# Performance work log

Measured on AMD Instinct MI355X. Metric: run time of the kernel, lower is better.

Reference implementation:

```python
import jax, jax.numpy as jnp
import numpy as np

B, N, IN, E, OUT = 4, 128, 256, 128, 128
EPS = 1e-5
NEG = -1.0e9


def _ln(x, s, o):
    m = x.mean(-1, keepdims=True)
    v = ((x - m) ** 2).mean(-1, keepdims=True)
    return s * jax.lax.rsqrt(v + EPS) * (x - m) + o


def setup_inputs() -> dict:
    key = jax.random.key(0)
    ks = jax.random.split(key, 30)

    def w(k, i, o):
        return (jax.random.normal(k, (i, o), jnp.float32) / np.sqrt(i)).astype(jnp.float32)

    z_dense = jax.random.normal(ks[0], (B, N, IN), jnp.float32)
    e_dense = jax.random.normal(ks[1], (B, N, N, E), jnp.float32)
    graph_fts = jax.random.normal(ks[2], (B, IN // 2), jnp.float32)
    lengths = jax.random.randint(ks[3], (B,), N // 2, N + 1)
    mask = jnp.arange(N)[None, :] < lengths[:, None]  # (B,N) bool
    adj = jax.random.uniform(ks[4], (B, N, N)) < 0.3
    adj = (adj | jnp.eye(N, dtype=bool)[None]) & mask[:, :, None] & mask[:, None, :]
    return dict(
        z_dense=z_dense, e_dense=e_dense, graph_fts=graph_fts, mask=mask, adj_mat=adj,
        Wt1=w(ks[5], IN, 8), Wt2=w(ks[6], IN, 8), Wt3=w(ks[7], IN, 8),
        We1=w(ks[8], E, 8), We2=w(ks[9], E, 8), We3=w(ks[10], E, 8),
        Wg=w(ks[11], IN // 2, 8),
        Wm1=w(ks[12], IN, OUT), Wm2=w(ks[13], IN, OUT), Wme=w(ks[14], E, OUT), Wmg=w(ks[15], E, OUT),
        ln1_s=jnp.ones((OUT,), jnp.float32), ln1_o=jnp.zeros((OUT,), jnp.float32),
        Wmlp1=w(ks[16], OUT, OUT),
        ln2_s=jnp.ones((OUT,), jnp.float32), ln2_o=jnp.zeros((OUT,), jnp.float32),
        Wmlp2=w(ks[17], OUT, OUT),
        WU1=w(ks[18], IN, OUT), WU2=w(ks[19], OUT, OUT), WU3=w(ks[20], 8, OUT),
        lnf_s=jnp.ones((OUT,), jnp.float32), lnf_o=jnp.zeros((OUT,), jnp.float32),
    )


def reference(z_dense, e_dense, graph_fts, mask, adj_mat,
              Wt1, Wt2, Wt3, We1, We2, We3, Wg,
              Wm1, Wm2, Wme, Wmg,
              ln1_s, ln1_o, Wmlp1, ln2_s, ln2_o, Wmlp2,
              WU1, WU2, WU3, lnf_s, lnf_o):
    mN = mask[..., None]  # (B,N,1)
    # --- triplet messages ---
    tri_1 = jnp.where(mN, z_dense @ Wt1, 0.0)  # (B,N,8)
    tri_2 = jnp.where(mN, z_dense @ Wt2, 0.0)
    tri_3 = jnp.where(mN, z_dense @ Wt3, 0.0)
    tri_e1 = e_dense @ We1  # (B,N,N,8)
    tri_e2 = e_dense @ We2
    tri_e3 = e_dense @ We3
    tri_g = graph_fts @ Wg  # (B,8)
    # (B,N,N,N,8) 7-way broadcast sum (axes: b, i, j, k)
    tri = (tri_1[:, :, None, None, :] + tri_2[:, None, :, None, :] + tri_3[:, None, None, :, :]
           + tri_e1[:, :, :, None, :] + tri_e2[:, :, None, :, :] + tri_e3[:, None, :, :, :]
           + tri_g[:, None, None, None, :])
    msk_tri = mask[:, None, None, :] | mask[:, None, :, None] | mask[:, :, None, None]
    tri = jnp.where(msk_tri[..., None], tri, NEG)
    tri_pooled = tri.max(axis=1)  # (B,N,N,8) -- max over first node axis
    tri_msgs = jax.nn.relu(tri_pooled @ WU3)  # (B,N,N,OUT)

    # --- pairwise messages ---
    msg_1 = jnp.where(mN, z_dense @ Wm1, 0.0)  # (B,N,OUT)
    msg_2 = jnp.where(mN, z_dense @ Wm2, 0.0)
    msg_e = jnp.where(adj_mat[..., None], e_dense @ Wme, 0.0)  # (B,N,N,OUT)
    msg_g = graph_fts @ Wmg  # (B,OUT)
    msgs = msg_1[:, None, :, :] + msg_2[:, :, None, :] + msg_e + msg_g[:, None, None, :]
    # M[-1]: [LN, ReLU, Linear] x2
    x = jax.nn.relu(_ln(msgs, ln1_s, ln1_o)) @ Wmlp1
    x = jax.nn.relu(_ln(x, ln2_s, ln2_o)) @ Wmlp2
    msgs = jnp.where(adj_mat[..., None], x, NEG).max(axis=1)  # (B,N,OUT)

    ret = _ln(z_dense @ WU1 + msgs @ WU2, lnf_s, lnf_o)  # (B,N,OUT)
    return ret, msgs, tri_msgs
```

## Files before the change

### kernel.cpp

```cpp
#include <hip/hip_runtime.h>

#define BN   4
#define NN   128
#define INF  256
#define EF   128
#define OUTF 128
#define EPSF 1e-5f
#define NEGF -998244352.0f

typedef __attribute__((ext_vector_type(8))) short short8;
typedef __attribute__((ext_vector_type(4))) float f32x4;

#define MFMA16(a, b, c) __builtin_amdgcn_mfma_f32_16x16x32_bf16(a, b, c, 0, 0, 0)

__device__ __forceinline__ unsigned short f2bf(float f) {
    unsigned u = __float_as_uint(f);
    u += 0x7fffu + ((u >> 16) & 1u);
    return (unsigned short)(u >> 16);
}
__device__ __forceinline__ unsigned pack2(float a, float b) {
    return (unsigned)f2bf(a) | ((unsigned)f2bf(b) << 16);
}

constexpr size_t TRI1 = 0;
constexpr size_t TRI2 = 4096;
constexpr size_t TRI3 = 8192;
constexpr size_t MSG1 = 12288;
constexpr size_t MSG2 = 77824;
constexpr size_t ZWU1 = 143360;
constexpr size_t TRIG = 208896;
constexpr size_t MSGG = 209920;
constexpr size_t E1T  = 210944;
constexpr size_t E2T  = 735232;
constexpr size_t E3N  = 1259520;
constexpr size_t PREPF = 1914880;

constexpr int W1T_OFF  = 0;
constexpr int W2T_OFF  = 16384;
constexpr int WMET_OFF = 32768;

constexpr size_t O_RET = 0;
constexpr size_t O_MSG = 65536;
constexpr size_t O_TRI = 131072;

__device__ __forceinline__ int detect_int(const void* mask) {
    const unsigned char* m = (const unsigned char*)mask;
    return (m[1] | m[2] | m[3]) == 0 ? 1 : 0;
}
__device__ __forceinline__ bool rdbool(const void* p, size_t idx, int isInt) {
    if (isInt) return ((const int*)p)[idx] != 0;
    return ((const unsigned char*)p)[idx] != 0;
}

__device__ __forceinline__ void stage_w(const unsigned short* __restrict__ prep, int offU,
                                        unsigned short* Wl, int w, int lane)
{
    const char* g = (const char*)(prep + offU) + w * 8192 + lane * 16;
    char* l = (char*)Wl + w * 8192;
    #pragma unroll
    for (int r = 0; r < 8; r++) {
        __builtin_amdgcn_global_load_lds(
            (const __attribute__((address_space(1))) void*)(g + r * 1024),
            (__attribute__((address_space(3))) void*)(l + r * 1024),
            16, 0, 0);
    }
}

__global__ __launch_bounds__(256, 4) void k_pre(
    const float* __restrict__ z, const float* __restrict__ e, const void* __restrict__ mask,
    const float* __restrict__ Wt1, const float* __restrict__ Wt2, const float* __restrict__ Wt3,
    const float* __restrict__ Wm1, const float* __restrict__ Wm2, const float* __restrict__ WU1,
    const float* __restrict__ g, const float* __restrict__ Wg, const float* __restrict__ Wmg,
    const float* __restrict__ W1, const float* __restrict__ W2, const float* __restrict__ Wme,
    const float* __restrict__ We1, const float* __restrict__ We2, const float* __restrict__ We3,
    float* __restrict__ ws, unsigned short* __restrict__ prep)
{
    int bx = blockIdx.x, tid = threadIdx.x;
    __shared__ __align__(16) unsigned char smem[128 * 136 * 2];

    if (bx < 512) {
        unsigned short* Ab = (unsigned short*)smem;
        int bi = bx;
        int b = bi >> 7, i = bi & 127;
        int lane = tid & 63, w = tid >> 6, q = lane >> 4, n = lane & 15;
        {
            int half = lane >> 5, c4 = (lane & 31) * 4;
            #pragma unroll
            for (int it = 0; it < 16; it++) {
                int row = 32 * w + 2 * it + half;
                float4 v = *(const float4*)(e + (size_t)bi * 16384 + (size_t)row * 128 + c4);
                unsigned* dst = (unsigned*)&Ab[row * 136 + c4];
                dst[0] = pack2(v.x, v.y);
                dst[1] = pack2(v.z, v.w);
            }
        }
        float t1v;
        {
            int c = lane & 7, kk = lane >> 3;
            const float* zr = z + (size_t)bi * INF;
            float s = 0.f;
            #pragma unroll
            for (int m = 0; m < 32; m++) s = fmaf(zr[kk * 32 + m], Wt1[(kk * 32 + m) * 8 + c], s);
            s += __shfl_xor(s, 8, 64);
            s += __shfl_xor(s, 16, 64);
            s += __shfl_xor(s, 32, 64);
            int isInt = detect_int(mask);
            t1v = rdbool(mask, bi, isInt) ? s : 0.f;
        }
        short8 bfrag[4][2];
        {
            #pragma unroll
            for (int t = 0; t < 2; t++) {
                int col = 16 * t + n;
                const float* Wsel = (col < 8) ? We1 : (col < 16 ? We2 : We3);
                int csel = col & 7;
                float mval = (col < 24) ? 1.f : 0.f;
                #pragma unroll
                for (int ks = 0; ks < 4; ks++) {
                    union { short8 s; unsigned short u[8]; } tmp;
                    #pragma unroll
                    for (int jj = 0; jj < 8; jj++) {
                        int k = ks * 32 + q * 8 + jj;
                        tmp.u[jj] = f2bf(Wsel[k * 8 + csel] * mval);
                    }
                    bfrag[ks][t] = tmp.s;
                }
            }
        }
        __builtin_amdgcn_wave_barrier();

        f32x4 ac2[2][2];
        #pragma unroll
        for (int rt = 0; rt < 2; rt++)
            #pragma unroll
            for (int t = 0; t < 2; t++) ac2[rt][t] = 0.f;
        #pragma unroll
        for (int ks = 0; ks < 4; ks++) {
            int k0 = ks * 32 + q * 8;
            short8 a0 = *(const short8*)&Ab[(32 * w + n) * 136 + k0];
            short8 a1 = *(const short8*)&Ab[(32 * w + 16 + n) * 136 + k0];
            #pragma unroll
            for (int t = 0; t < 2; t++) {
                ac2[0][t] = MFMA16(a0, bfrag[ks][t], ac2[0][t]);
                ac2[1][t] = MFMA16(a1, bfrag[ks][t], ac2[1][t]);
            }
        }
        #pragma unroll
        for (int rt = 0; rt < 2; rt++)
            #pragma unroll
            for (int reg = 0; reg < 4; reg++) {
                int row = 32 * w + 16 * rt + 4 * q + reg;
                float v0 = ac2[rt][0][reg];
                if (n < 8) ws[E1T + ((size_t)(b * 128 + row) * 128 + i) * 8 + n] = v0 + t1v;
                else       ws[E2T + ((size_t)(b * 128 + row) * 128 + i) * 8 + (n - 8)] = v0;
                if (n < 8) ws[E3N + ((size_t)bi * 128 + row) * 8 + n] = ac2[rt][1][reg];
            }
        return;
    }
    if (bx < 1024) {
        int bn = bx - 512;
        int isInt = detect_int(mask);
        float* zr = (float*)smem;
        zr[tid] = z[(size_t)bn * INF + tid];
        __syncthreads();
        float mk = rdbool(mask, bn, isInt) ? 1.f : 0.f;
        for (int idx = tid; idx < 408; idx += 256) {
            const float* W; int c; size_t dst; int width; bool msk;
            if (idx < 8)        { W = Wt1; c = idx;       dst = TRI1 + (size_t)bn * 8;   width = 8;   msk = true;  }
            else if (idx < 16)  { W = Wt2; c = idx - 8;   dst = TRI2 + (size_t)bn * 8;   width = 8;   msk = true;  }
            else if (idx < 24)  { W = Wt3; c = idx - 16;  dst = TRI3 + (size_t)bn * 8;   width = 8;   msk = true;  }
            else if (idx < 152) { W = Wm1; c = idx - 24;  dst = MSG1 + (size_t)bn * 128; width = 128; msk = true;  }
            else if (idx < 280) { W = Wm2; c = idx - 152; dst = MSG2 + (size_t)bn * 128; width = 128; msk = true;  }
            else                { W = WU1; c = idx - 280; dst = ZWU1 + (size_t)bn * 128; width = 128; msk = false; }
            float a0 = 0.f, a1 = 0.f;
            #pragma unroll 8
            for (int k = 0; k < INF; k += 2) {
                a0 += zr[k] * W[k * width + c];
                a1 += zr[k + 1] * W[(k + 1) * width + c];
            }
            float acc = a0 + a1;
            ws[dst + c] = msk ? acc * mk : acc;
        }
        return;
    }
    if (bx < 1028) {
        int b = bx - 1024;
        float* gr = (float*)smem;
        if (tid < 128) gr[tid] = g[b * 128 + tid];
        __syncthreads();
        if (tid < 8) {
            float a = 0.f;
            for (int k = 0; k < 128; k++) a += gr[k] * Wg[k * 8 + tid];
            ws[TRIG + b * 8 + tid] = a;
        } else if (tid >= 128) {
            int c = tid - 128;
            float a = 0.f;
            for (int k = 0; k < 128; k++) a += gr[k] * Wmg[k * 128 + c];
            ws[MSGG + b * 128 + c] = a;
        }
        return;
    }
    {
        int idx = (bx - 1028) * 256 + tid;
        const float* W = (idx < 16384) ? W1 : (idx < 32768 ? W2 : Wme);
        int local = idx & 16383;
        int f = local >> 3, jj = local & 7;
        int lane = f & 63, fg = f >> 6;
        int t = fg & 7, ks = fg >> 3;
        int n = lane & 15, q = lane >> 4;
        int row = 16 * t + n;
        int k = ks * 32 + q * 8 + jj;
        prep[idx] = f2bf(W[k * 128 + row]);
    }
}

#define PAIR_GEMM_L do {                                                       \
    _Pragma("unroll")                                                          \
    for (int ks = 0; ks < 4; ks++) {                                           \
        int kf = ks * 32 + q * 8;                                              \
        short8 a0 = *(const short8*)&Ab[(32 * w + n) * 136 + kf];              \
        short8 a1 = *(const short8*)&Ab[(32 * w + 16 + n) * 136 + kf];         \
        _Pragma("unroll")                                                      \
        for (int t = 0; t < 8; t++) {                                          \
            short8 bt = *(const short8*)&Wl[((ks * 8 + t) * 64 + lane) * 8];   \
            acc[0][t] = MFMA16(a0, bt, acc[0][t]);                             \
            acc[1][t] = MFMA16(a1, bt, acc[1][t]);                             \
        }                                                                      \
    }                                                                          \
} while (0)

__global__ __launch_bounds__(256, 2) void k_main(
    const float* __restrict__ e, const void* __restrict__ mask, const void* __restrict__ adj,
    const float* __restrict__ ln1s, const float* __restrict__ ln1o,
    const float* __restrict__ ln2s, const float* __restrict__ ln2o,
    const unsigned short* __restrict__ prep, const float* __restrict__ WU3,
    float* __restrict__ ws, float* __restrict__ out)
{
    int bx = blockIdx.x, tid = threadIdx.x;
    __shared__ __align__(16) unsigned char smem[128 * 136 * 2 + 2048 + 32768];
    int lane = tid & 63, w = tid >> 6, q = lane >> 4, n = lane & 15;
    int isInt = detect_int(mask);

    if (bx < 256) {
        int g = bx;
        int j0 = ((g >> 3) & 7) * 16, k0 = (g & 7) * 16, b = g >> 6;
        int wi = w >> 1, wc = w & 1;
        int tj = lane >> 3, tk = lane & 7;
        int col4 = (tid & 31) * 4, rowgrp = tid >> 5;

        int lenb;
        {
            unsigned long long m0 = __ballot(rdbool(mask, (size_t)b * 128 + lane, isInt));
            unsigned long long m1 = __ballot(rdbool(mask, (size_t)b * 128 + 64 + lane, isInt));
            lenb = __popcll(m0) + __popcll(m1);
        }
        bool needU = (j0 + 15 >= lenb) && (k0 + 15 >= lenb);

        float* Pb = (float*)smem + w * 1152;
        float* Qb = Pb + 576;

        f32x4 aM[2][2];
        #pragma unroll
        for (int jj = 0; jj < 2; jj++)
            #pragma unroll
            for (int kk = 0; kk < 2; kk++) aM[jj][kk] = NEGF;

        if (!needU) {
            for (int ch = 0; ch < 8; ch++) {
                int ibase = wi * 64 + ch * 8;
                #pragma unroll
                for (int r = 0; r < 2; r++) {
                    int f = r * 64 + lane;
                    int jr = f >> 3, ii = f & 7;
                    f32x4 pv = *(const f32x4*)(ws + E1T + (size_t)(b * 128 + j0 + jr) * 1024 + (ibase + ii) * 8 + wc * 4);
                    f32x4 qv = *(const f32x4*)(ws + E2T + (size_t)(b * 128 + k0 + jr) * 1024 + (ibase + ii) * 8 + wc * 4);
                    *(f32x4*)(Pb + jr * 36 + ii * 4) = pv;
                    *(f32x4*)(Qb + jr * 36 + ii * 4) = qv;
                }
                __builtin_amdgcn_wave_barrier();
                #pragma unroll
                for (int ii = 0; ii < 8; ii++) {
                    f32x4 p0 = *(const f32x4*)(Pb + tj * 36 + ii * 4);
                    f32x4 p1 = *(const f32x4*)(Pb + (tj + 8) * 36 + ii * 4);
                    f32x4 q0 = *(const f32x4*)(Qb + tk * 36 + ii * 4);
                    f32x4 q1 = *(const f32x4*)(Qb + (tk + 8) * 36 + ii * 4);
                    aM[0][0] = __builtin_elementwise_max(aM[0][0], p0 + q0);
                    aM[0][1] = __builtin_elementwise_max(aM[0][1], p0 + q1);
                    aM[1][0] = __builtin_elementwise_max(aM[1][0], p1 + q0);
                    aM[1][1] = __builtin_elementwise_max(aM[1][1], p1 + q1);
                }
            }
        } else {
            f32x4 aU[2][2];
            #pragma unroll
            for (int jj = 0; jj < 2; jj++)
                #pragma unroll
                for (int kk = 0; kk < 2; kk++) aU[jj][kk] = NEGF;
            unsigned long long mball = __ballot(rdbool(mask, (size_t)b * 128 + wi * 64 + lane, isInt));
            for (int ch = 0; ch < 8; ch++) {
                int ibase = wi * 64 + ch * 8;
                #pragma unroll
                for (int r = 0; r < 2; r++) {
                    int f = r * 64 + lane;
                    int jr = f >> 3, ii = f & 7;
                    f32x4 pv = *(const f32x4*)(ws + E1T + (size_t)(b * 128 + j0 + jr) * 1024 + (ibase + ii) * 8 + wc * 4);
                    f32x4 qv = *(const f32x4*)(ws + E2T + (size_t)(b * 128 + k0 + jr) * 1024 + (ibase + ii) * 8 + wc * 4);
                    *(f32x4*)(Pb + jr * 36 + ii * 4) = pv;
                    *(f32x4*)(Qb + jr * 36 + ii * 4) = qv;
                }
                __builtin_amdgcn_wave_barrier();
                #pragma unroll
                for (int ii = 0; ii < 8; ii++) {
                    f32x4 p0 = *(const f32x4*)(Pb + tj * 36 + ii * 4);
                    f32x4 p1 = *(const f32x4*)(Pb + (tj + 8) * 36 + ii * 4);
                    f32x4 q0 = *(const f32x4*)(Qb + tk * 36 + ii * 4);
                    f32x4 q1 = *(const f32x4*)(Qb + (tk + 8) * 36 + ii * 4);
                    f32x4 v00 = p0 + q0, v01 = p0 + q1, v10 = p1 + q0, v11 = p1 + q1;
                    if ((mball >> (ch * 8 + ii)) & 1) {
                        aM[0][0] = __builtin_elementwise_max(aM[0][0], v00);
                        aM[0][1] = __builtin_elementwise_max(aM[0][1], v01);
                        aM[1][0] = __builtin_elementwise_max(aM[1][0], v10);
                        aM[1][1] = __builtin_elementwise_max(aM[1][1], v11);
                    } else {
                        aU[0][0] = __builtin_elementwise_max(aU[0][0], v00);
                        aU[0][1] = __builtin_elementwise_max(aU[0][1], v01);
                        aU[1][0] = __builtin_elementwise_max(aU[1][0], v10);
                        aU[1][1] = __builtin_elementwise_max(aU[1][1], v11);
                    }
                }
            }
            bool mj[2], mk2[2];
            mj[0]  = (j0 + tj)     < lenb;
            mj[1]  = (j0 + tj + 8) < lenb;
            mk2[0] = (k0 + tk)     < lenb;
            mk2[1] = (k0 + tk + 8) < lenb;
            #pragma unroll
            for (int jj = 0; jj < 2; jj++)
                #pragma unroll
                for (int kk = 0; kk < 2; kk++)
                    if (mj[jj] | mk2[kk])
                        aM[jj][kk] = __builtin_elementwise_max(aM[jj][kk], aU[jj][kk]);
        }
        __syncthreads();
        float* pooled = (float*)smem;
        float4 wvr[8];
        #pragma unroll
        for (int c = 0; c < 8; c++) wvr[c] = *(const float4*)(WU3 + c * 128 + col4);

        if (wi == 0) {
            #pragma unroll
            for (int jj = 0; jj < 2; jj++)
                #pragma unroll
                for (int kk = 0; kk < 2; kk++) {
                    int p = (tj + 8 * jj) * 16 + (tk + 8 * kk);
                    #pragma unroll
                    for (int cc = 0; cc < 4; cc++)
                        pooled[(wc * 4 + cc) * 260 + p] = aM[jj][kk][cc];
                }
        }
        __syncthreads();
        if (wi == 1) {
            const float* tg = ws + TRIG + (size_t)b * 8 + wc * 4;
            #pragma unroll
            for (int jj = 0; jj < 2; jj++)
                #pragma unroll
                for (int kk = 0; kk < 2; kk++) {
                    int jv = j0 + tj + 8 * jj, kv = k0 + tk + 8 * kk;
                    const float* t2 = ws + TRI2 + (size_t)(b * 128 + jv) * 8 + wc * 4;
                    const float* t3 = ws + TRI3 + (size_t)(b * 128 + kv) * 8 + wc * 4;
                    const float* e3 = ws + E3N + ((size_t)(b * 128 + jv) * 128 + kv) * 8 + wc * 4;
                    int p = (tj + 8 * jj) * 16 + (tk + 8 * kk);
                    #pragma unroll
                    for (int cc = 0; cc < 4; cc++) {
                        int idx = (wc * 4 + cc) * 260 + p;
                        pooled[idx] = fmaxf(pooled[idx], aM[jj][kk][cc]) + t2[cc] + t3[cc] + e3[cc] + tg[cc];
                    }
                }
        }
        __syncthreads();
        #pragma unroll
        for (int pass = 0; pass < 32; pass++) {
            int p = pass * 8 + rowgrp;
            float4 s = { 0.f, 0.f, 0.f, 0.f };
            #pragma unroll
            for (int c = 0; c < 8; c++) {
                float pv = pooled[c * 260 + p];
                s.x += pv * wvr[c].x; s.y += pv * wvr[c].y;
                s.z += pv * wvr[c].z; s.w += pv * wvr[c].w;
            }
            s.x = fmaxf(s.x, 0.f); s.y = fmaxf(s.y, 0.f);
            s.z = fmaxf(s.z, 0.f); s.w = fmaxf(s.w, 0.f);
            int pj = p >> 4, pk = p & 15;
            *(float4*)(out + O_TRI + ((size_t)(b * 128 + j0 + pj) * 128 + (k0 + pk)) * 128 + col4) = s;
        }
        return;
    }

    unsigned short* Ab = (unsigned short*)smem;
    float* pw = (float*)(smem + 128 * 136 * 2);
    unsigned short* Wl = (unsigned short*)(smem + 128 * 136 * 2 + 2048);
    int bj = bx - 256;
    int b = bj >> 7, j = bj & 127;

    int lenb;
    {
        unsigned long long m0 = __ballot(rdbool(mask, (size_t)b * 128 + lane, isInt));
        unsigned long long m1 = __ballot(rdbool(mask, (size_t)b * 128 + 64 + lane, isInt));
        lenb = __popcll(m0) + __popcll(m1);
    }
    if (j >= lenb) {
        if (tid < 128) out[O_MSG + (size_t)bj * 128 + tid] = NEGF;
        return;
    }

    bool waveActive = (32 * w) < lenb;

    stage_w(prep, WMET_OFF, Wl, w, lane);
    if (waveActive) {
        int half = lane >> 5, c4 = (lane & 31) * 4;
        #pragma unroll
        for (int it = 0; it < 16; it++) {
            int row = 32 * w + 2 * it + half;
            float4 v = *(const float4*)(e + (((size_t)b * 128 + row) * 128 + j) * 128 + c4);
            unsigned* dst = (unsigned*)&Ab[row * 136 + c4];
            dst[0] = pack2(v.x, v.y);
            dst[1] = pack2(v.z, v.w);
        }
    }
    __syncthreads();

    float colmax[8];
    #pragma unroll
    for (int t = 0; t < 8; t++) colmax[t] = NEGF;
    float adjm[2][4];
    f32x4 acc[2][8];

    if (waveActive) {
        #pragma unroll
        for (int rt = 0; rt < 2; rt++)
            #pragma unroll
            for (int t = 0; t < 8; t++) acc[rt][t] = 0.f;
        PAIR_GEMM_L;
    }
    __syncthreads();
    stage_w(prep, W1T_OFF, Wl, w, lane);

    if (waveActive) {
        float msum[8];
        #pragma unroll
        for (int t = 0; t < 8; t++)
            msum[t] = ws[MSG1 + (size_t)bj * 128 + 16 * t + n] + ws[MSGG + (size_t)b * 128 + 16 * t + n];
        float rs[2][4], rss[2][4];
        #pragma unroll
        for (int rt = 0; rt < 2; rt++)
            #pragma unroll
            for (int reg = 0; reg < 4; reg++) {
                int row = 32 * w + 16 * rt + 4 * q + reg;
                bool av = rdbool(adj, ((size_t)b * 128 + row) * 128 + j, isInt);
                adjm[rt][reg] = av ? 1.f : 0.f;
                float s = 0.f, ssq = 0.f;
                #pragma unroll
                for (int t = 0; t < 8; t++) {
                    float v = acc[rt][t][reg] * adjm[rt][reg]
                            + ws[MSG2 + ((size_t)b * 128 + row) * 128 + 16 * t + n] + msum[t];
                    acc[rt][t][reg] = v;
                    s += v; ssq += v * v;
                }
                rs[rt][reg] = s; rss[rt][reg] = ssq;
            }
        #pragma unroll
        for (int d = 1; d < 16; d <<= 1) {
            #pragma unroll
            for (int rt = 0; rt < 2; rt++)
                #pragma unroll
                for (int reg = 0; reg < 4; reg++) {
                    rs[rt][reg]  += __shfl_xor(rs[rt][reg], d, 64);
                    rss[rt][reg] += __shfl_xor(rss[rt][reg], d, 64);
                }
        }
        float s1v[8], o1v[8];
        #pragma unroll
        for (int t = 0; t < 8; t++) { s1v[t] = ln1s[16 * t + n]; o1v[t] = ln1o[16 * t + n]; }
        #pragma unroll
        for (int rt = 0; rt < 2; rt++)
            #pragma unroll
            for (int reg = 0; reg < 4; reg++) {
                float mu = rs[rt][reg] * (1.f / 128);
                float inv = rsqrtf(rss[rt][reg] * (1.f / 128) - mu * mu + EPSF);
                int row = 32 * w + 16 * rt + 4 * q + reg;
                #pragma unroll
                for (int t = 0; t < 8; t++) {
                    float v = fmaxf(s1v[t] * inv * (acc[rt][t][reg] - mu) + o1v[t], 0.f);
                    Ab[row * 136 + 16 * t + n] = f2bf(v);
                }
            }
    }
    __syncthreads();

    if (waveActive) {
        #pragma unroll
        for (int rt = 0; rt < 2; rt++)
            #pragma unroll
            for (int t = 0; t < 8; t++) acc[rt][t] = 0.f;
        PAIR_GEMM_L;
    }
    __syncthreads();
    stage_w(prep, W2T_OFF, Wl, w, lane);

    if (waveActive) {
        float rs[2][4], rss[2][4];
        #pragma unroll
        for (int rt = 0; rt < 2; rt++)
            #pragma unroll
            for (int reg = 0; reg < 4; reg++) {
                float s = 0.f, ssq = 0.f;
                #pragma unroll
                for (int t = 0; t < 8; t++) { float v = acc[rt][t][reg]; s += v; ssq += v * v; }
                rs[rt][reg] = s; rss[rt][reg] = ssq;
            }
        #pragma unroll
        for (int d = 1; d < 16; d <<= 1) {
            #pragma unroll
            for (int rt = 0; rt < 2; rt++)
                #pragma unroll
                for (int reg = 0; reg < 4; reg++) {
                    rs[rt][reg]  += __shfl_xor(rs[rt][reg], d, 64);
                    rss[rt][reg] += __shfl_xor(rss[rt][reg], d, 64);
                }
        }
        float s2v[8], o2v[8];
        #pragma unroll
        for (int t = 0; t < 8; t++) { s2v[t] = ln2s[16 * t + n]; o2v[t] = ln2o[16 * t + n]; }
        #pragma unroll
        for (int rt = 0; rt < 2; rt++)
            #pragma unroll
            for (int reg = 0; reg < 4; reg++) {
                float mu = rs[rt][reg] * (1.f / 128);
                float inv = rsqrtf(rss[rt][reg] * (1.f / 128) - mu * mu + EPSF);
                int row = 32 * w + 16 * rt + 4 * q + reg;
                #pragma unroll
                for (int t = 0; t < 8; t++) {
                    float v = fmaxf(s2v[t] * inv * (acc[rt][t][reg] - mu) + o2v[t], 0.f);
                    Ab[row * 136 + 16 * t + n] = f2bf(v);
                }
            }
    }
    __syncthreads();

    if (waveActive) {
        #pragma unroll
        for (int rt = 0; rt < 2; rt++)
            #pragma unroll
            for (int t = 0; t < 8; t++) acc[rt][t] = 0.f;
        PAIR_GEMM_L;

        #pragma unroll
        for (int rt = 0; rt < 2; rt++)
            #pragma unroll
            for (int reg = 0; reg < 4; reg++) {
                if (adjm[rt][reg] > 0.f) {
                    #pragma unroll
                    for (int t = 0; t < 8; t++) colmax[t] = fmaxf(colmax[t], acc[rt][t][reg]);
                }
            }
    }
    #pragma unroll
    for (int t = 0; t < 8; t++) {
        colmax[t] = fmaxf(colmax[t], __shfl_xor(colmax[t], 16, 64));
        colmax[t] = fmaxf(colmax[t], __shfl_xor(colmax[t], 32, 64));
    }
    if (lane < 16) {
        #pragma unroll
        for (int t = 0; t < 8; t++) pw[w * 128 + 16 * t + lane] = colmax[t];
    }
    __syncthreads();
    if (tid < 128) {
        float mx = fmaxf(fmaxf(pw[tid], pw[128 + tid]), fmaxf(pw[256 + tid], pw[384 + tid]));
        out[O_MSG + (size_t)bj * 128 + tid] = mx;
    }
}

__global__ __launch_bounds__(128) void k_final(
    const float* __restrict__ ws, const float* __restrict__ WU2,
    const float* __restrict__ lnfs, const float* __restrict__ lnfo,
    float* __restrict__ out)
{
    int bn = blockIdx.x, tid = threadIdx.x;
    __shared__ float mrow[128];
    __shared__ float red[4];
    mrow[tid] = out[O_MSG + (size_t)bn * 128 + tid];
    __syncthreads();
    float y = ws[ZWU1 + (size_t)bn * 128 + tid];
    float a0 = 0.f, a1 = 0.f;
    #pragma unroll 8
    for (int k = 0; k < 128; k += 2) {
        a0 = fmaf(mrow[k], WU2[k * 128 + tid], a0);
        a1 = fmaf(mrow[k + 1], WU2[(k + 1) * 128 + tid], a1);
    }
    y += a0 + a1;
    float s = y, ss = y * y;
    for (int d = 1; d < 64; d <<= 1) { s += __shfl_xor(s, d, 64); ss += __shfl_xor(ss, d, 64); }
    if ((tid & 63) == 0) { red[(tid >> 6) * 2] = s; red[(tid >> 6) * 2 + 1] = ss; }
    __syncthreads();
    float S = red[0] + red[2], SS = red[1] + red[3];
    float m_ = S * (1.f / 128), v_ = SS * (1.f / 128) - m_ * m_;
    float r = rsqrtf(v_ + EPSF);
    out[O_RET + (size_t)bn * 128 + tid] = lnfs[tid] * r * (y - m_) + lnfo[tid];
}

extern "C" void kernel_launch(void* const* d_in, const int* in_sizes, int n_in,
                              void* d_out, int out_size, void* d_ws, size_t ws_size,
                              hipStream_t stream)
{
    const float* z    = (const float*)d_in[0];
    const float* e    = (const float*)d_in[1];
    const float* gf   = (const float*)d_in[2];
    const void*  mask = d_in[3];
    const void*  adj  = d_in[4];
    const float* Wt1 = (const float*)d_in[5];
    const float* Wt2 = (const float*)d_in[6];
    const float* Wt3 = (const float*)d_in[7];
    const float* We1 = (const float*)d_in[8];
    const float* We2 = (const float*)d_in[9];
    const float* We3 = (const float*)d_in[10];
    const float* Wg  = (const float*)d_in[11];
    const float* Wm1 = (const float*)d_in[12];
    const float* Wm2 = (const float*)d_in[13];
    const float* Wme = (const float*)d_in[14];
    const float* Wmg = (const float*)d_in[15];
    const float* ln1s = (const float*)d_in[16];
    const float* ln1o = (const float*)d_in[17];
    const float* W1   = (const float*)d_in[18];
    const float* ln2s = (const float*)d_in[19];
    const float* ln2o = (const float*)d_in[20];
    const float* W2   = (const float*)d_in[21];
    const float* WU1  = (const float*)d_in[22];
    const float* WU2  = (const float*)d_in[23];
    const float* WU3  = (const float*)d_in[24];
    const float* lnfs = (const float*)d_in[25];
    const float* lnfo = (const float*)d_in[26];
    float* out = (float*)d_out;
    float* ws  = (float*)d_ws;
    unsigned short* prep = (unsigned short*)(ws + PREPF);

    hipLaunchKernelGGL(k_pre, dim3(1220), dim3(256), 0, stream,
                       z, e, mask, Wt1, Wt2, Wt3, Wm1, Wm2, WU1, gf, Wg, Wmg,
                       W1, W2, Wme, We1, We2, We3, ws, prep);
    hipLaunchKernelGGL(k_main, dim3(768), dim3(256), 0, stream,
                       e, mask, adj, ln1s, ln1o, ln2s, ln2o, prep, WU3, ws, out);
    hipLaunchKernelGGL(k_final, dim3(512), dim3(128), 0, stream,
                       ws, WU2, lnfs, lnfo, out);
}
```

Measured before the change: 181.5 us.

## Halve LDS weight buffer by staging weights in two K-halves to raise occupancy

The k_main pairwise path now stages each 128x128 bf16 weight matrix into LDS in two 16KB halves instead of one 32KB buffer. This cuts shared memory per block from about 69KB to 52KB and raises the launch bound from 2 to 3 blocks per CU. The cost is extra __syncthreads and a serialized reload between the two K-halves of each GEMM, which exposes global-to-LDS latency that was previously covered.

```diff
diff --git a/kernel.cpp b/kernel.cpp
--- a/kernel.cpp
+++ b/kernel.cpp
@@ -52,13 +52,13 @@
     return ((const unsigned char*)p)[idx] != 0;
 }
 
-__device__ __forceinline__ void stage_w(const unsigned short* __restrict__ prep, int offU,
+__device__ __forceinline__ void stage_h(const unsigned short* __restrict__ prep, int offU,
                                         unsigned short* Wl, int w, int lane)
 {
-    const char* g = (const char*)(prep + offU) + w * 8192 + lane * 16;
-    char* l = (char*)Wl + w * 8192;
+    const char* g = (const char*)(prep + offU) + w * 4096 + lane * 16;
+    char* l = (char*)Wl + w * 4096;
     #pragma unroll
-    for (int r = 0; r < 8; r++) {
+    for (int r = 0; r < 4; r++) {
         __builtin_amdgcn_global_load_lds(
             (const __attribute__((address_space(1))) void*)(g + r * 1024),
             (__attribute__((address_space(3))) void*)(l + r * 1024),
@@ -214,22 +214,22 @@
     }
 }
 
-#define PAIR_GEMM_L do {                                                       \
+#define PAIR_GEMM_H(HS) do {                                                   \
     _Pragma("unroll")                                                          \
-    for (int ks = 0; ks < 4; ks++) {                                           \
-        int kf = ks * 32 + q * 8;                                              \
+    for (int ls = 0; ls < 2; ls++) {                                           \
+        int kf = (2 * (HS) + ls) * 32 + q * 8;                                 \
         short8 a0 = *(const short8*)&Ab[(32 * w + n) * 136 + kf];              \
         short8 a1 = *(const short8*)&Ab[(32 * w + 16 + n) * 136 + kf];         \
         _Pragma("unroll")                                                      \
         for (int t = 0; t < 8; t++) {                                          \
-            short8 bt = *(const short8*)&Wl[((ks * 8 + t) * 64 + lane) * 8];   \
+            short8 bt = *(const short8*)&Wl[((ls * 8 + t) * 64 + lane) * 8];   \
             acc[0][t] = MFMA16(a0, bt, acc[0][t]);                             \
             acc[1][t] = MFMA16(a1, bt, acc[1][t]);                             \
         }                                                                      \
     }                                                                          \
 } while (0)
 
-__global__ __launch_bounds__(256, 2) void k_main(
+__global__ __launch_bounds__(256, 3) void k_main(
     const float* __restrict__ e, const void* __restrict__ mask, const void* __restrict__ adj,
     const float* __restrict__ ln1s, const float* __restrict__ ln1o,
     const float* __restrict__ ln2s, const float* __restrict__ ln2o,
@@ -237,7 +237,7 @@
     float* __restrict__ ws, float* __restrict__ out)
 {
     int bx = blockIdx.x, tid = threadIdx.x;
-    __shared__ __align__(16) unsigned char smem[128 * 136 * 2 + 2048 + 32768];
+    __shared__ __align__(16) unsigned char smem[53248];
     int lane = tid & 63, w = tid >> 6, q = lane >> 4, n = lane & 15;
     int isInt = detect_int(mask);
 
@@ -397,8 +397,8 @@
     }
 
     unsigned short* Ab = (unsigned short*)smem;
-    float* pw = (float*)(smem + 128 * 136 * 2);
-    unsigned short* Wl = (unsigned short*)(smem + 128 * 136 * 2 + 2048);
+    float* pw = (float*)(smem + 34816);
+    unsigned short* Wl = (unsigned short*)(smem + 36864);
     int bj = bx - 256;
     int b = bj >> 7, j = bj & 127;
 
@@ -415,7 +415,7 @@
 
     bool waveActive = (32 * w) < lenb;
 
-    stage_w(prep, WMET_OFF, Wl, w, lane);
+    stage_h(prep, WMET_OFF, Wl, w, lane);
     if (waveActive) {
         int half = lane >> 5, c4 = (lane & 31) * 4;
         #pragma unroll
@@ -435,15 +435,17 @@
     float adjm[2][4];
     f32x4 acc[2][8];
 
-    if (waveActive) {
-        #pragma unroll
-        for (int rt = 0; rt < 2; rt++)
-            #pragma unroll
-            for (int t = 0; t < 8; t++) acc[rt][t] = 0.f;
-        PAIR_GEMM_L;
-    }
-    __syncthreads();
-    stage_w(prep, W1T_OFF, Wl, w, lane);
+    #pragma unroll
+    for (int rt = 0; rt < 2; rt++)
+        #pragma unroll
+        for (int t = 0; t < 8; t++) acc[rt][t] = 0.f;
+    if (waveActive) PAIR_GEMM_H(0);
+    __syncthreads();
+    stage_h(prep, WMET_OFF + 8192, Wl, w, lane);
+    __syncthreads();
+    if (waveActive) PAIR_GEMM_H(1);
+    __syncthreads();
+    stage_h(prep, W1T_OFF, Wl, w, lane);
 
     if (waveActive) {
         float msum[8];
@@ -497,15 +499,17 @@
     }
     __syncthreads();
 
-    if (waveActive) {
-        #pragma unroll
-        for (int rt = 0; rt < 2; rt++)
-            #pragma unroll
-            for (int t = 0; t < 8; t++) acc[rt][t] = 0.f;
-        PAIR_GEMM_L;
-    }
-    __syncthreads();
-    stage_w(prep, W2T_OFF, Wl, w, lane);
+    #pragma unroll
+    for (int rt = 0; rt < 2; rt++)
+        #pragma unroll
+        for (int t = 0; t < 8; t++) acc[rt][t] = 0.f;
+    if (waveActive) PAIR_GEMM_H(0);
+    __syncthreads();
+    stage_h(prep, W1T_OFF + 8192, Wl, w, lane);
+    __syncthreads();
+    if (waveActive) PAIR_GEMM_H(1);
+    __syncthreads();
+    stage_h(prep, W2T_OFF, Wl, w, lane);
 
     if (waveActive) {
         float rs[2][4], rss[2][4];
@@ -547,13 +551,16 @@
     }
     __syncthreads();
 
+    #pragma unroll
+    for (int rt = 0; rt < 2; rt++)
+        #pragma unroll
+        for (int t = 0; t < 8; t++) acc[rt][t] = 0.f;
+    if (waveActive) PAIR_GEMM_H(0);
+    __syncthreads();
+    stage_h(prep, W2T_OFF + 8192, Wl, w, lane);
+    __syncthreads();
     if (waveActive) {
-        #pragma unroll
-        for (int rt = 0; rt < 2; rt++)
-            #pragma unroll
-            for (int t = 0; t < 8; t++) acc[rt][t] = 0.f;
-        PAIR_GEMM_L;
-
+        PAIR_GEMM_H(1);
         #pragma unroll
         for (int rt = 0; rt < 2; rt++)
             #pragma unroll
```

Measured after the change: 179.3 us. About the same (-1.2%).
